# Kernel optimization log

Hardware: AMD Instinct MI355X
Metric: run time of the kernel (lower is better)

## Reference

```python
import jax, jax.numpy as jnp
import numpy as np

N_NODES = 50000
N_EDGES = 800000
IN_NF = 64
OUT_NF = 64
HID = 128
H = 4
D = 64
HD = H * D
EDGE_IN = 2 * IN_NF + 1 + 6   # 135
MSG_IN = HID + 1 + 3 + 6      # 138


def _p(key, i, shape, scale=0.02):
    return scale * jax.random.normal(jax.random.fold_in(key, i), shape, dtype=jnp.float32)


def setup_inputs() -> dict:
    key = jax.random.key(0)
    ks = jax.random.split(key, 4)
    inp = {
        "h": jax.random.normal(ks[0], (N_NODES, IN_NF), dtype=jnp.float32),
        "x": jax.random.normal(ks[1], (N_NODES, 3), dtype=jnp.float32),
        "edge_index": jax.random.randint(ks[2], (2, N_EDGES), 0, N_NODES, dtype=jnp.int32),
        "mask": jnp.ones((N_EDGES,), dtype=bool),
    }
    pk = jax.random.fold_in(key, 7)
    i = iter(range(100))
    inp.update({
        "Wq": _p(pk, next(i), (IN_NF, HD)), "bq": jnp.zeros((HD,)),
        "Wk": _p(pk, next(i), (IN_NF, HD)), "bk": jnp.zeros((HD,)),
        "Wv": _p(pk, next(i), (IN_NF, HD)), "bv": jnp.zeros((HD,)),
        "Wo": _p(pk, next(i), (HD, OUT_NF)), "bo": jnp.zeros((OUT_NF,)),
        "pw1": _p(pk, next(i), (1, HID // 2)), "pb1": jnp.zeros((HID // 2,)),
        "pw2": _p(pk, next(i), (HID // 2, H)), "pb2": jnp.zeros((H,)),
        "ew1": _p(pk, next(i), (EDGE_IN, HID)), "eb1": jnp.zeros((HID,)),
        "ew2": _p(pk, next(i), (HID, HID)), "eb2": jnp.zeros((HID,)),
        "eww": _p(pk, next(i), (HID, H)), "ewb": jnp.zeros((H,)),
        "mw1": _p(pk, next(i), (MSG_IN, HID)), "mb1": jnp.zeros((HID,)),
        "mw2": _p(pk, next(i), (HID, HID)), "mb2": jnp.zeros((HID,)),
        "gw": _p(pk, next(i), (HID, H)), "gb": jnp.zeros((H,)),
        "cw1": _p(pk, next(i), (HID, HID)), "cb1": jnp.zeros((HID,)),
        "cw2": _p(pk, next(i), (HID, H)), "cb2": jnp.zeros((H,)),
        "coord_weights": jnp.ones((H,)),
        "xw1": _p(pk, next(i), (HID, HID)), "xb1": jnp.zeros((HID,)),
        "xw2": _p(pk, next(i), (HID, H)), "xb2": jnp.zeros((H,)),
    })
    return inp


def reference(h, x, edge_index, mask,
              Wq, bq, Wk, bk, Wv, bv, Wo, bo,
              pw1, pb1, pw2, pb2,
              ew1, eb1, ew2, eb2, eww, ewb,
              mw1, mb1, mw2, mb2,
              gw, gb, cw1, cb1, cw2, cb2,
              coord_weights, xw1, xb1, xw2, xb2):
    silu = jax.nn.silu
    row, col = edge_index[0], edge_index[1]
    n = h.shape[0]

    q = (h @ Wq + bq).reshape(n, H, D)
    k = (h @ Wk + bk).reshape(n, H, D)
    v = (h @ Wv + bv).reshape(n, H, D)

    rel_pos = x[row] - x[col]                         # [E,3]
    rel_dist = jnp.sum(rel_pos ** 2, -1, keepdims=True)  # [E,1]
    pos_enc = silu(rel_dist @ pw1 + pb1) @ pw2 + pb2     # [E,H]

    # torch .std() is unbiased (ddof=1)
    xn = (x - x.mean(0, keepdims=True)) / (jnp.std(x, 0, keepdims=True, ddof=1) + 1e-8)

    edge_attr = jnp.concatenate([h[row], h[col], rel_dist, xn[row], xn[col]], -1)
    ef = silu(edge_attr @ ew1 + eb1) @ ew2 + eb2      # [E,HID]
    ewt = ef @ eww + ewb                              # [E,H]

    attn = jnp.einsum('ehd,ehd->eh', q[row], k[col]) / jnp.sqrt(jnp.float32(D))
    attn = attn + pos_enc + ewt
    attn = jnp.where(mask[:, None], attn, jnp.float32(-1e9))

    amax = jax.ops.segment_max(attn, row, num_segments=n)   # [N,H]
    attn = jnp.exp(attn - amax[row])
    asum = jax.ops.segment_sum(attn, row, num_segments=n)
    attn = attn / (asum[row] + 1e-8)                         # [E,H]

    msg_in = jnp.concatenate([ef, attn.mean(1, keepdims=True), rel_pos, xn[row], xn[col]], -1)
    msgs = silu(msg_in @ mw1 + mb1) @ mw2 + mb2              # [E,HID]

    gates = jax.nn.sigmoid(msgs @ gw + gb)                   # [E,H]
    cwts = silu(msgs @ cw1 + cb1) @ cw2 + cb2                # [E,H]

    # per-head index_add into the same buffer == sum over heads of the scalar weight
    s = jnp.sum(gates * cwts * coord_weights, -1, keepdims=True)  # [E,1]
    base = 0.9 * rel_pos + 0.1 * x[col]
    coord_update = jax.ops.segment_sum(s * base / (n - 1), row, num_segments=n)

    cross_v = jnp.cross(rel_pos, jnp.roll(rel_pos, 1, axis=0))
    cg = silu(msgs @ xw1 + xb1) @ xw2 + xb2                  # [E,H]
    cross_s = jnp.sum(cg, -1, keepdims=True)
    coord_update = coord_update + jax.ops.segment_sum(cross_s * cross_v / (n - 1), row, num_segments=n)

    wv = jax.ops.segment_sum(attn[..., None] * v[col], row, num_segments=n)  # [N,H,D]
    out = wv.reshape(n, HD) @ Wo + bo
    return out, coord_update
```

## Files before the change

### kernel.cpp

```cpp
#include <hip/hip_runtime.h>
#include <hip/hip_bf16.h>

#define NN 50000
#define NE 800000

typedef __bf16 bf16x8 __attribute__((ext_vector_type(8)));
typedef float f4v __attribute__((ext_vector_type(4)));

__device__ __forceinline__ float silu_f(float v){
  return v*__builtin_amdgcn_rcpf(1.0f+__expf(-v));
}
__device__ __forceinline__ float bf2f(unsigned int u){ return __uint_as_float(u<<16); }
__device__ __forceinline__ unsigned bfr(float f){
  unsigned b = __float_as_uint(f);
  return b + 0x7fffu + ((b>>16)&1u);
}
__device__ __forceinline__ unsigned short f2bf(float f){ return (unsigned short)(bfr(f)>>16); }
__device__ __forceinline__ unsigned pk2(float a, float b){
  unsigned r;
  asm("v_cvt_pk_bf16_f32 %0, %1, %2" : "=v"(r) : "v"(a), "v"(b));
  return r;
}

union U8 { unsigned short us[8]; uint4 u4; };

__device__ __forceinline__ void pack8(unsigned short* dst, float4 a, float4 b){
  uint4 u;
  u.x = pk2(a.x,a.y); u.y = pk2(a.z,a.w);
  u.z = pk2(b.x,b.y); u.w = pk2(b.z,b.w);
  *(uint4*)dst = u;
}

__device__ __forceinline__ int lidx(int e, int c, int CH){
  return (e*CH + ((c & ~7) | ((c ^ e) & 7))) << 3;
}

template<int KC, int CH>
__device__ __forceinline__ void gemm_rm(const unsigned short* act, const unsigned short* wf,
                                        int wu, int lane, f4v (&acc)[4][2]){
  int le = lane & 15, quad = lane >> 4;
  #pragma unroll
  for (int kc=0;kc<KC;kc++){
    bf16x8 a0 = *(const bf16x8*)(wf + (((wu*2  )*KC + kc)<<9) + lane*8);
    bf16x8 a1 = *(const bf16x8*)(wf + (((wu*2+1)*KC + kc)<<9) + lane*8);
    int chunk = kc*4 + quad;
    #pragma unroll
    for (int et=0;et<4;et++){
      bf16x8 b = *(const bf16x8*)(act + lidx(et*16+le, chunk, CH));
      acc[et][0] = __builtin_amdgcn_mfma_f32_16x16x32_bf16(a0, b, acc[et][0], 0,0,0);
      acc[et][1] = __builtin_amdgcn_mfma_f32_16x16x32_bf16(a1, b, acc[et][1], 0,0,0);
    }
  }
}

template<int CH, bool SILU, bool BIAS>
__device__ __forceinline__ void epi_rm(unsigned short* dst, const f4v (&acc)[4][2],
                                       const float* bias, int wu, int lane){
  int le = lane & 15, quad = lane >> 4;
  #pragma unroll
  for (int ot=0; ot<2; ot++){
    float4 bv = make_float4(0,0,0,0);
    if (BIAS) bv = *(const float4*)(bias + wu*32 + ot*16 + quad*4);
    int chunk = wu*4 + ot*2 + (quad>>1);
    int soff = (quad&1)*4;
    #pragma unroll
    for (int et=0; et<4; et++){
      float v0=acc[et][ot][0], v1=acc[et][ot][1], v2=acc[et][ot][2], v3=acc[et][ot][3];
      if (BIAS){ v0+=bv.x; v1+=bv.y; v2+=bv.z; v3+=bv.w; }
      if (SILU){ v0=silu_f(v0); v1=silu_f(v1); v2=silu_f(v2); v3=silu_f(v3); }
      uint2 u; u.x = pk2(v0,v1); u.y = pk2(v2,v3);
      *(uint2*)(dst + lidx(et*16+le, chunk, CH) + soff) = u;
    }
  }
}

template<int CH>
__device__ __forceinline__ void mfma_head(const unsigned short* buf, const unsigned short* whf,
                                          int wu, int lane, float* dst ){
  int le = lane & 15, quad = lane >> 4;
  f4v hacc = {0.f,0.f,0.f,0.f};
  #pragma unroll
  for (int kc=0;kc<4;kc++){
    bf16x8 a = *(const bf16x8*)(whf + (kc<<9) + lane*8);
    bf16x8 b = *(const bf16x8*)(buf + lidx(wu*16+le, kc*4+quad, CH));
    hacc = __builtin_amdgcn_mfma_f32_16x16x32_bf16(a, b, hacc, 0,0,0);
  }
  if (quad==0){
    #pragma unroll
    for (int r=0;r<4;r++) dst[r*65 + wu*16 + le] = hacc[r];
  }
}

__global__ __launch_bounds__(256) void k_zero(float* __restrict__ p, int n){
  int i = blockIdx.x*256 + threadIdx.x;
  if (i < n) p[i] = 0.f;
}

__global__ __launch_bounds__(256) void k_wcomb(const float* __restrict__ ew2, const float* __restrict__ eww,
                                               const float* __restrict__ eb2, const float* __restrict__ ewb,
                                               const float* __restrict__ pb2,
                                               float* __restrict__ wcomb, float* __restrict__ stats){
  int t = threadIdx.x;
  #pragma unroll
  for (int o=t;o<512;o+=256){
    int i=o>>2, hh=o&3;
    float s=0.f;
    for (int j=0;j<128;j++) s += ew2[i*128+j]*eww[j*4+hh];
    wcomb[o]=s;
  }
  if (t<4){
    float s=0.f;
    for (int j=0;j<128;j++) s += eb2[j]*eww[j*4+t];
    stats[12+t] = s + ewb[t] + pb2[t];
  }
}

__global__ __launch_bounds__(256) void k_wprep(const float* __restrict__ src, unsigned short* __restrict__ dst,
                                               int Kreal, int KC){
  int idx = blockIdx.x*256 + threadIdx.x;
  int tot = 8*KC*512;
  if (idx >= tot) return;
  int nt  = idx/(KC*512); int rem = idx%(KC*512);
  int kc  = rem>>9;       int r2  = rem&511;
  int lq  = r2>>3;        int j   = r2&7;
  int k   = kc*32 + (lq>>4)*8 + j;
  int n   = nt*16 + (lq&15);
  float v = (k < Kreal) ? src[k*128 + n] : 0.f;
  dst[idx] = f2bf(v);
}

__global__ __launch_bounds__(256) void k_wprepq(const float* __restrict__ src, unsigned short* __restrict__ dst){
  int idx = blockIdx.x*256 + threadIdx.x;
  if (idx >= 16384) return;
  int nt  = idx>>10;  int rem = idx&1023;
  int kc  = rem>>9;   int r2  = rem&511;
  int lq  = r2>>3;    int j   = r2&7;
  int k   = kc*32 + (lq>>4)*8 + j;
  int n   = nt*16 + (lq&15);
  dst[idx] = f2bf(src[k*256 + n]);
}

__global__ __launch_bounds__(256) void k_wprep4(const float* __restrict__ src, unsigned short* __restrict__ dst){
  int idx = blockIdx.x*256 + threadIdx.x;
  if (idx >= 2048) return;
  int kc = idx>>9; int r2 = idx&511; int lq = r2>>3; int j = r2&7;
  int k = kc*32 + (lq>>4)*8 + j;
  int n = lq&15;
  dst[idx] = f2bf((n<4) ? src[k*4+n] : 0.f);
}

__global__ __launch_bounds__(256) void k_stats(const float* __restrict__ x, float* __restrict__ stats){
  int i = blockIdx.x*256 + threadIdx.x;
  float v0=0.f,v1=0.f,v2=0.f;
  if (i < NN){ v0=x[i*3+0]; v1=x[i*3+1]; v2=x[i*3+2]; }
  float vals[6] = {v0,v1,v2,v0*v0,v1*v1,v2*v2};
  __shared__ float red[256];
  for (int c=0;c<6;c++){
    red[threadIdx.x]=vals[c];
    __syncthreads();
    for (int off=128; off>0; off>>=1){
      if (threadIdx.x < off) red[threadIdx.x] += red[threadIdx.x+off];
      __syncthreads();
    }
    if (threadIdx.x==0) atomicAdd(&stats[c], red[0]);
    __syncthreads();
  }
}

__global__ __launch_bounds__(64) void k_statsfin(float* __restrict__ stats){
  int t = threadIdx.x;
  if (t < 3){
    float s = stats[t], sq = stats[3+t];
    float mean = s/(float)NN;
    float var = (sq - s*s/(float)NN)/(float)(NN-1);
    float sd = sqrtf(var);
    stats[6+t] = mean;
    stats[9+t] = 1.0f/(sd + 1e-8f);
  }
}

__global__ __launch_bounds__(256) void k_qkv2(const float* __restrict__ h,
    const unsigned short* __restrict__ wqf,
    const float* __restrict__ bq, const float* __restrict__ bk, const float* __restrict__ bv,
    unsigned short* __restrict__ q, unsigned short* __restrict__ kk, unsigned short* __restrict__ v){
  __shared__ __align__(16) unsigned short hstage[64*8*8];
  int t = threadIdx.x; int lane = t & 63; int w = t >> 6;
  int wu = __builtin_amdgcn_readfirstlane(w);
  int r0 = blockIdx.x*64;
  {
    int row = r0 + lane;
    float4 a = make_float4(0,0,0,0), b2 = make_float4(0,0,0,0),
           c = make_float4(0,0,0,0), d2 = make_float4(0,0,0,0);
    if (row < NN){
      const float* hr = h + (size_t)row*64 + wu*16;
      a  = *(const float4*)(hr);    b2 = *(const float4*)(hr+4);
      c  = *(const float4*)(hr+8);  d2 = *(const float4*)(hr+12);
    }
    pack8(&hstage[lidx(lane, 2*wu,   8)], a, b2);
    pack8(&hstage[lidx(lane, 2*wu+1, 8)], c, d2);
  }
  __syncthreads();
  int le = lane & 15, quad = lane >> 4;
  #pragma unroll
  for (int ti=0; ti<12; ti++){
    int tt = ti*4 + wu;
    f4v acc[4];
    f4v z = {0.f,0.f,0.f,0.f};
    acc[0]=z; acc[1]=z; acc[2]=z; acc[3]=z;
    #pragma unroll
    for (int kc=0;kc<2;kc++){
      bf16x8 a = *(const bf16x8*)(wqf + ((tt*2 + kc)<<9) + lane*8);
      int chunk = kc*4 + quad;
      #pragma unroll
      for (int et=0;et<4;et++){
        bf16x8 b = *(const bf16x8*)(hstage + lidx(et*16+le, chunk, 8));
        acc[et] = __builtin_amdgcn_mfma_f32_16x16x32_bf16(a, b, acc[et], 0,0,0);
      }
    }
    int mat = tt>>4; int ct = tt&15;
    const float* bias = (mat==0)? bq : (mat==1)? bk : bv;
    unsigned short* outp = (mat==0)? q : (mat==1)? kk : v;
    float4 bv4 = *(const float4*)(bias + ct*16 + quad*4);
    int col = ct*16 + quad*4;
    #pragma unroll
    for (int et=0;et<4;et++){
      int row2 = r0 + et*16 + le;
      if (row2 < NN){
        float v0=acc[et][0]+bv4.x, v1=acc[et][1]+bv4.y, v2=acc[et][2]+bv4.z, v3=acc[et][3]+bv4.w;
        if (mat<2){
          uint2 u; u.x = pk2(v0,v1); u.y = pk2(v2,v3);
          *(uint2*)(outp + (size_t)row2*256 + col) = u;
        } else {
          int head = col>>6, dd = col&63;
          unsigned short* vp = outp + (size_t)row2*256 + (size_t)dd*4 + head;
          vp[0]  = f2bf(v0);
          vp[4]  = f2bf(v1);
          vp[8]  = f2bf(v2);
          vp[12] = f2bf(v3);
        }
      }
    }
  }
}

__global__ __launch_bounds__(256) void k_count(const int* __restrict__ ei, int* __restrict__ counts){
  int e = blockIdx.x*256 + threadIdx.x;
  if (e < NE) atomicAdd(&counts[ei[e]], 1);
}

__global__ __launch_bounds__(256) void k_scan(int* __restrict__ counts, int* __restrict__ offs){
  __shared__ int ps[256];
  int t = threadIdx.x;
  int base = t*196;
  int s = 0;
  for (int i=0;i<196;i++){ int idx = base+i; if (idx < NN) s += counts[idx]; }
  ps[t]=s; __syncthreads();
  for (int off=1; off<256; off<<=1){
    int vv = (t>=off)? ps[t-off] : 0;
    __syncthreads();
    ps[t]+=vv;
    __syncthreads();
  }
  int run = ps[t]-s;
  for (int i=0;i<196;i++){
    int idx = base+i;
    if (idx < NN){ int c = counts[idx]; offs[idx]=run; counts[idx]=run; run+=c; }
  }
  if (t==255) offs[NN]=run;
}

__global__ __launch_bounds__(256) void k_fill(const int* __restrict__ ei, int* __restrict__ cursor, int* __restrict__ elist){
  int e = blockIdx.x*256 + threadIdx.x;
  if (e < NE){
    int r = ei[e];
    int p = atomicAdd(&cursor[r],1);
    elist[p] = e;
  }
}

__global__ __launch_bounds__(256) void k_e1(
    const float* __restrict__ h, const float* __restrict__ x, const int* __restrict__ ei,
    const float* __restrict__ stats,
    const unsigned short* __restrict__ qb, const unsigned short* __restrict__ kb,
    const unsigned short* __restrict__ wfrag, const unsigned short* __restrict__ whfrag,
    const float* __restrict__ eb1,
    const float* __restrict__ pw1, const float* __restrict__ pb1,
    const float* __restrict__ pw2,
    float* __restrict__ asum, float* __restrict__ eattn){
  __shared__ __align__(16) unsigned short bufIn[64*24*8];
  __shared__ float logit_s[256];
  __shared__ float ewt2_s[4*65];
  __shared__ float pos_s[4*65];
  __shared__ float rd_s[64], xnr_s[192], xnc_s[192];
  __shared__ int row_s[64], col_s[64];
  int t = threadIdx.x; int lane = t & 63; int w = t >> 6;
  int wu = __builtin_amdgcn_readfirstlane(w);
  int ebase = blockIdx.x * 64;

  for (int i=t;i<260;i+=256) pos_s[i]=0.f;
  if (t < 64){
    int ge = ebase + t;
    int r = ei[ge], c = ei[NE+ge];
    row_s[t]=r; col_s[t]=c;
    float xr0=x[r*3],xr1=x[r*3+1],xr2=x[r*3+2];
    float xc0=x[c*3],xc1=x[c*3+1],xc2=x[c*3+2];
    float rp0=xr0-xc0, rp1=xr1-xc1, rp2=xr2-xc2;
    rd_s[t]=rp0*rp0+rp1*rp1+rp2*rp2;
    float m0=stats[6],m1=stats[7],m2=stats[8],s0=stats[9],s1=stats[10],s2=stats[11];
    xnr_s[t*3+0]=(xr0-m0)*s0; xnr_s[t*3+1]=(xr1-m1)*s1; xnr_s[t*3+2]=(xr2-m2)*s2;
    xnc_s[t*3+0]=(xc0-m0)*s0; xnc_s[t*3+1]=(xc1-m1)*s1; xnc_s[t*3+2]=(xc2-m2)*s2;
  }
  __syncthreads();

  for (int ii=0; ii<16; ii++){
    int e = wu*16+ii;
    int r = row_s[e], c = col_s[e];
    uint2 qu = *(const uint2*)(qb + (size_t)r*256 + lane*4);
    uint2 ku = *(const uint2*)(kb + (size_t)c*256 + lane*4);
    float d = bf2f(qu.x&0xffffu)*bf2f(ku.x&0xffffu)
            + bf2f(qu.x>>16)   *bf2f(ku.x>>16)
            + bf2f(qu.y&0xffffu)*bf2f(ku.y&0xffffu)
            + bf2f(qu.y>>16)   *bf2f(ku.y>>16);
    d += __shfl_xor(d,1,16); d += __shfl_xor(d,2,16);
    d += __shfl_xor(d,4,16); d += __shfl_xor(d,8,16);
    if ((lane&15)==0) logit_s[e*4 + (lane>>4)] = d*0.125f;
  }
  {
    int jb = wu*16;
    float rd = rd_s[lane];
    float p0=0,p1=0,p2=0,p3=0;
    for (int j=jb; j<jb+16; j++){
      float hp = rd*pw1[j] + pb1[j];
      float hs = silu_f(hp);
      const float4 w4 = *(const float4*)(pw2 + j*4);
      p0+=hs*w4.x; p1+=hs*w4.y; p2+=hs*w4.z; p3+=hs*w4.w;
    }
    atomicAdd(&pos_s[0*65+lane],p0);
    atomicAdd(&pos_s[1*65+lane],p1);
    atomicAdd(&pos_s[2*65+lane],p2);
    atomicAdd(&pos_s[3*65+lane],p3);
  }
  {
    const float* hr = h + (size_t)row_s[lane]*64 + wu*16;
    pack8(&bufIn[lidx(lane, 2*wu,   24)], *(const float4*)(hr),   *(const float4*)(hr+4));
    pack8(&bufIn[lidx(lane, 2*wu+1, 24)], *(const float4*)(hr+8), *(const float4*)(hr+12));
    const float* hc = h + (size_t)col_s[lane]*64 + wu*16;
    pack8(&bufIn[lidx(lane, 8+2*wu, 24)], *(const float4*)(hc),   *(const float4*)(hc+4));
    pack8(&bufIn[lidx(lane, 9+2*wu, 24)], *(const float4*)(hc+8), *(const float4*)(hc+12));
  }
  if (t < 64){
    pack8(&bufIn[lidx(t,16,24)],
          make_float4(rd_s[t], xnr_s[t*3+0], xnr_s[t*3+1], xnr_s[t*3+2]),
          make_float4(xnc_s[t*3+0], xnc_s[t*3+1], xnc_s[t*3+2], 0.f));
  }
  {
    uint4 z4 = make_uint4(0,0,0,0);
    int e = t&63, j = t>>6;
    if (j < 3) *(uint4*)&bufIn[lidx(e, 17+j, 24)] = z4;
  }
  __syncthreads();
  f4v acc[4][2];
  f4v z = {0.f,0.f,0.f,0.f};
  #pragma unroll
  for (int et=0;et<4;et++){ acc[et][0]=z; acc[et][1]=z; }
  gemm_rm<5,24>(bufIn, wfrag + 0, wu, lane, acc);
  __syncthreads();
  epi_rm<24,true,true>(bufIn, acc, eb1, wu, lane);
  __syncthreads();
  mfma_head<24>(bufIn, whfrag + 0, wu, lane, ewt2_s);
  __syncthreads();
  {
    int e2 = t>>2, hh = t&3;
    float lg = logit_s[t] + stats[12+hh] + ewt2_s[hh*65+e2] + pos_s[hh*65+e2];
    float ex = __expf(lg);
    eattn[(size_t)ebase*4 + t] = ex;
    atomicAdd(&asum[row_s[e2]*4 + hh], ex);
  }
}

__global__ __launch_bounds__(256) void k_e2(
    const float* __restrict__ h, const float* __restrict__ x, const int* __restrict__ ei,
    const float* __restrict__ stats,
    const float* __restrict__ asum, const float* __restrict__ eattn,
    const unsigned short* __restrict__ wfrag, const unsigned short* __restrict__ whfrag,
    const float* __restrict__ eb1, const float* __restrict__ eb2,
    const float* __restrict__ mb1, const float* __restrict__ mb2,
    const float* __restrict__ gb,
    const float* __restrict__ cb1, const float* __restrict__ cb2,
    const float* __restrict__ coordw,
    const float* __restrict__ xb1, const float* __restrict__ xb2,
    float* __restrict__ cvec){
  __shared__ __align__(16) unsigned short bufIn[64*24*8];
  __shared__ __align__(16) unsigned short bufA [64*16*8];
  __shared__ float attn_s[256];
  __shared__ float g_s[4*65], c_s[4*65], xx_s[4*65];
  __shared__ float s_s[64], cs_s[64];
  __shared__ float rp_s[192], rd_s[64], xnr_s[192], xnc_s[192], xc_s[192];
  __shared__ int row_s[64], col_s[64];
  int t = threadIdx.x; int lane = t & 63; int w = t >> 6;
  int wu = __builtin_amdgcn_readfirstlane(w);
  int ebase = blockIdx.x * 64;

  if (t < 64){
    int ge = ebase + t;
    int r = ei[ge], c = ei[NE+ge];
    row_s[t]=r; col_s[t]=c;
    float xr0=x[r*3],xr1=x[r*3+1],xr2=x[r*3+2];
    float xc0=x[c*3],xc1=x[c*3+1],xc2=x[c*3+2];
    float rp0=xr0-xc0, rp1=xr1-xc1, rp2=xr2-xc2;
    rp_s[t*3+0]=rp0; rp_s[t*3+1]=rp1; rp_s[t*3+2]=rp2;
    rd_s[t]=rp0*rp0+rp1*rp1+rp2*rp2;
    xc_s[t*3+0]=xc0; xc_s[t*3+1]=xc1; xc_s[t*3+2]=xc2;
    float m0=stats[6],m1=stats[7],m2=stats[8],s0=stats[9],s1=stats[10],s2=stats[11];
    xnr_s[t*3+0]=(xr0-m0)*s0; xnr_s[t*3+1]=(xr1-m1)*s1; xnr_s[t*3+2]=(xr2-m2)*s2;
    xnc_s[t*3+0]=(xc0-m0)*s0; xnc_s[t*3+1]=(xc1-m1)*s1; xnc_s[t*3+2]=(xc2-m2)*s2;
  }
  __syncthreads();
  {
    int e2 = t>>2; int hh = t&3;
    float ex = eattn[(size_t)ebase*4 + t];
    float a = ex / (asum[row_s[e2]*4 + hh] + 1e-8f);
    attn_s[t]=a;
  }
  {
    const float* hr = h + (size_t)row_s[lane]*64 + wu*16;
    pack8(&bufIn[lidx(lane, 2*wu,   24)], *(const float4*)(hr),   *(const float4*)(hr+4));
    pack8(&bufIn[lidx(lane, 2*wu+1, 24)], *(const float4*)(hr+8), *(const float4*)(hr+12));
    const float* hc = h + (size_t)col_s[lane]*64 + wu*16;
    pack8(&bufIn[lidx(lane, 8+2*wu, 24)], *(const float4*)(hc),   *(const float4*)(hc+4));
    pack8(&bufIn[lidx(lane, 9+2*wu, 24)], *(const float4*)(hc+8), *(const float4*)(hc+12));
  }
  if (t < 64){
    pack8(&bufIn[lidx(t,16,24)],
          make_float4(rd_s[t], xnr_s[t*3+0], xnr_s[t*3+1], xnr_s[t*3+2]),
          make_float4(xnc_s[t*3+0], xnc_s[t*3+1], xnc_s[t*3+2], 0.f));
  }
  {
    uint4 z4 = make_uint4(0,0,0,0);
    int e = t&63, j = t>>6;
    *(uint4*)&bufIn[lidx(e, 17+j, 24)] = z4;
    if (j < 3) *(uint4*)&bufIn[lidx(e, 21+j, 24)] = z4;
  }
  __syncthreads();
  f4v acc[4][2];
  f4v z = {0.f,0.f,0.f,0.f};
  #pragma unroll
  for (int et=0;et<4;et++){ acc[et][0]=z; acc[et][1]=z; }
  gemm_rm<5,24>(bufIn, wfrag + 0, wu, lane, acc);
  epi_rm<16,true,true>(bufA, acc, eb1, wu, lane);
  __syncthreads();
  #pragma unroll
  for (int et=0;et<4;et++){ acc[et][0]=z; acc[et][1]=z; }
  gemm_rm<4,16>(bufA, wfrag + 20480, wu, lane, acc);
  epi_rm<24,false,true>(bufIn, acc, eb2, wu, lane);
  if (t < 64){
    float am = 0.25f*(attn_s[t*4]+attn_s[t*4+1]+attn_s[t*4+2]+attn_s[t*4+3]);
    pack8(&bufIn[lidx(t,16,24)],
          make_float4(am, rp_s[t*3+0], rp_s[t*3+1], rp_s[t*3+2]),
          make_float4(xnr_s[t*3+0], xnr_s[t*3+1], xnr_s[t*3+2], xnc_s[t*3+0]));
    pack8(&bufIn[lidx(t,17,24)],
          make_float4(xnc_s[t*3+1], xnc_s[t*3+2], 0.f, 0.f),
          make_float4(0.f,0.f,0.f,0.f));
  }
  __syncthreads();
  #pragma unroll
  for (int et=0;et<4;et++){ acc[et][0]=z; acc[et][1]=z; }
  gemm_rm<5,24>(bufIn, wfrag + 36864, wu, lane, acc);
  epi_rm<16,true,true>(bufA, acc, mb1, wu, lane);
  __syncthreads();
  #pragma unroll
  for (int et=0;et<4;et++){ acc[et][0]=z; acc[et][1]=z; }
  gemm_rm<4,16>(bufA, wfrag + 57344, wu, lane, acc);
  epi_rm<24,false,true>(bufIn, acc, mb2, wu, lane);
  __syncthreads();
  mfma_head<24>(bufIn, whfrag + 2048, wu, lane, g_s);
  f4v ax[4][2];
  #pragma unroll
  for (int et=0;et<4;et++){ acc[et][0]=z; acc[et][1]=z; ax[et][0]=z; ax[et][1]=z; }
  {
    const unsigned short* wfc = wfrag + 73728;
    const unsigned short* wfx = wfrag + 90112;
    int le = lane&15, quad = lane>>4;
    #pragma unroll
    for (int kc=0;kc<4;kc++){
      bf16x8 ac0 = *(const bf16x8*)(wfc + (((wu*2  )*4 + kc)<<9) + lane*8);
      bf16x8 ac1 = *(const bf16x8*)(wfc + (((wu*2+1)*4 + kc)<<9) + lane*8);
      bf16x8 ax0 = *(const bf16x8*)(wfx + (((wu*2  )*4 + kc)<<9) + lane*8);
      bf16x8 ax1 = *(const bf16x8*)(wfx + (((wu*2+1)*4 + kc)<<9) + lane*8);
      int chunk = kc*4 + quad;
      #pragma unroll
      for (int et=0;et<4;et++){
        bf16x8 b = *(const bf16x8*)(bufIn + lidx(et*16+le, chunk, 24));
        acc[et][0] = __builtin_amdgcn_mfma_f32_16x16x32_bf16(ac0, b, acc[et][0], 0,0,0);
        acc[et][1] = __builtin_amdgcn_mfma_f32_16x16x32_bf16(ac1, b, acc[et][1], 0,0,0);
        ax[et][0]  = __builtin_amdgcn_mfma_f32_16x16x32_bf16(ax0, b, ax[et][0], 0,0,0);
        ax[et][1]  = __builtin_amdgcn_mfma_f32_16x16x32_bf16(ax1, b, ax[et][1], 0,0,0);
      }
    }
  }
  __syncthreads();
  epi_rm<16,true,true>(bufA, acc, cb1, wu, lane);
  epi_rm<24,true,true>(bufIn, ax, xb1, wu, lane);
  __syncthreads();
  mfma_head<16>(bufA, whfrag + 4096, wu, lane, c_s);
  mfma_head<24>(bufIn, whfrag + 6144, wu, lane, xx_s);
  __syncthreads();
  {
    int e2 = t>>2; int hh = t&3;
    float g = __builtin_amdgcn_rcpf(1.0f+__expf(-(g_s[hh*65+e2]+gb[hh])));
    float cwv = c_s[hh*65+e2]+cb2[hh];
    float sv = g*cwv*coordw[hh];
    float csv = xx_s[hh*65+e2]+xb2[hh];
    sv += __shfl_xor(sv,1);  sv += __shfl_xor(sv,2);
    csv += __shfl_xor(csv,1); csv += __shfl_xor(csv,2);
    if (hh==0){ s_s[e2]=sv; cs_s[e2]=csv; }
  }
  __syncthreads();
  if (t < 64){
    int ge = ebase + t;
    float rp0=rp_s[t*3],rp1=rp_s[t*3+1],rp2=rp_s[t*3+2];
    float pp0,pp1,pp2;
    if (t > 0){ pp0=rp_s[(t-1)*3]; pp1=rp_s[(t-1)*3+1]; pp2=rp_s[(t-1)*3+2]; }
    else {
      int gp = (ebase==0)? (NE-1) : (ebase-1);
      int rr=ei[gp], cc2=ei[NE+gp];
      pp0=x[rr*3]-x[cc2*3]; pp1=x[rr*3+1]-x[cc2*3+1]; pp2=x[rr*3+2]-x[cc2*3+2];
    }
    float cv0 = rp1*pp2 - rp2*pp1;
    float cv1 = rp2*pp0 - rp0*pp2;
    float cv2 = rp0*pp1 - rp1*pp0;
    float sv = s_s[t], csv = cs_s[t];
    const float inv = 1.0f/49999.0f;
    cvec[(size_t)ge*3+0] = (sv*(0.9f*rp0+0.1f*xc_s[t*3+0]) + csv*cv0)*inv;
    cvec[(size_t)ge*3+1] = (sv*(0.9f*rp1+0.1f*xc_s[t*3+1]) + csv*cv1)*inv;
    cvec[(size_t)ge*3+2] = (sv*(0.9f*rp2+0.1f*xc_s[t*3+2]) + csv*cv2)*inv;
  }
}

__global__ __launch_bounds__(256) void k_aggout(
    const int* __restrict__ ei, const int* __restrict__ offs, const int* __restrict__ elist,
    const float* __restrict__ eattn, const unsigned short* __restrict__ vb,
    const float* __restrict__ cvec, const float* __restrict__ Wo, const float* __restrict__ bo,
    const float* __restrict__ asum,
    float* __restrict__ outp){
  __shared__ float wvs[4*256];
  int t = threadIdx.x; int lane = t & 63; int w = t >> 6;
  int node = blockIdx.x*4 + w;
  const int* colp = ei + NE;
  int s0 = offs[node], s1 = offs[node+1];
  float a0=0,a1=0,a2=0,a3=0,cc=0;
  int i = s0;
  for (; i+4<=s1; i+=4){
    int e0=elist[i], e1=elist[i+1], e2=elist[i+2], e3=elist[i+3];
    int c0=colp[e0], c1=colp[e1], c2=colp[e2], c3=colp[e3];
    uint2 v0 = *(const uint2*)(vb + (size_t)c0*256 + lane*4);
    uint2 v1 = *(const uint2*)(vb + (size_t)c1*256 + lane*4);
    uint2 v2 = *(const uint2*)(vb + (size_t)c2*256 + lane*4);
    uint2 v3 = *(const uint2*)(vb + (size_t)c3*256 + lane*4);
    float4 at0 = *(const float4*)(eattn + (size_t)e0*4);
    float4 at1 = *(const float4*)(eattn + (size_t)e1*4);
    float4 at2 = *(const float4*)(eattn + (size_t)e2*4);
    float4 at3 = *(const float4*)(eattn + (size_t)e3*4);
    if (lane < 3) cc += cvec[(size_t)e0*3+lane] + cvec[(size_t)e1*3+lane]
                      + cvec[(size_t)e2*3+lane] + cvec[(size_t)e3*3+lane];
    a0 += at0.x*bf2f(v0.x&0xffffu) + at1.x*bf2f(v1.x&0xffffu) + at2.x*bf2f(v2.x&0xffffu) + at3.x*bf2f(v3.x&0xffffu);
    a1 += at0.y*bf2f(v0.x>>16)     + at1.y*bf2f(v1.x>>16)     + at2.y*bf2f(v2.x>>16)     + at3.y*bf2f(v3.x>>16);
    a2 += at0.z*bf2f(v0.y&0xffffu) + at1.z*bf2f(v1.y&0xffffu) + at2.z*bf2f(v2.y&0xffffu) + at3.z*bf2f(v3.y&0xffffu);
    a3 += at0.w*bf2f(v0.y>>16)     + at1.w*bf2f(v1.y>>16)     + at2.w*bf2f(v2.y>>16)     + at3.w*bf2f(v3.y>>16);
  }
  for (; i<s1; i++){
    int e0 = elist[i];
    int c0 = colp[e0];
    uint2 v0 = *(const uint2*)(vb + (size_t)c0*256 + lane*4);
    float4 at0 = *(const float4*)(eattn + (size_t)e0*4);
    if (lane < 3) cc += cvec[(size_t)e0*3+lane];
    a0 += at0.x*bf2f(v0.x&0xffffu);
    a1 += at0.y*bf2f(v0.x>>16);
    a2 += at0.z*bf2f(v0.y&0xffffu);
    a3 += at0.w*bf2f(v0.y>>16);
  }
  {
    const float* as = asum + (size_t)node*4;
    a0 /= (as[0] + 1e-8f);
    a1 /= (as[1] + 1e-8f);
    a2 /= (as[2] + 1e-8f);
    a3 /= (as[3] + 1e-8f);
  }
  wvs[w*256 +       lane]=a0;
  wvs[w*256 +  64 + lane]=a1;
  wvs[w*256 + 128 + lane]=a2;
  wvs[w*256 + 192 + lane]=a3;
  if (lane < 3) outp[(size_t)NN*64 + (size_t)node*3 + lane] = cc;
  float o = bo[lane];
  #pragma unroll 4
  for (int k2=0;k2<256;k2++) o += wvs[w*256+k2] * Wo[k2*64+lane];
  outp[(size_t)node*64 + lane] = o;
}

extern "C" void kernel_launch(void* const* d_in, const int* in_sizes, int n_in,
                              void* d_out, int out_size, void* d_ws, size_t ws_size,
                              hipStream_t stream) {
  const float* h  = (const float*)d_in[0];
  const float* x  = (const float*)d_in[1];
  const int*   ei = (const int*)d_in[2];
  const float* Wq=(const float*)d_in[4];  const float* bq=(const float*)d_in[5];
  const float* Wk=(const float*)d_in[6];  const float* bk=(const float*)d_in[7];
  const float* Wv=(const float*)d_in[8];  const float* bv=(const float*)d_in[9];
  const float* Wo=(const float*)d_in[10]; const float* bo=(const float*)d_in[11];
  const float* pw1=(const float*)d_in[12]; const float* pb1=(const float*)d_in[13];
  const float* pw2=(const float*)d_in[14]; const float* pb2=(const float*)d_in[15];
  const float* ew1=(const float*)d_in[16]; const float* eb1=(const float*)d_in[17];
  const float* ew2=(const float*)d_in[18]; const float* eb2=(const float*)d_in[19];
  const float* eww=(const float*)d_in[20]; const float* ewb=(const float*)d_in[21];
  const float* mw1=(const float*)d_in[22]; const float* mb1=(const float*)d_in[23];
  const float* mw2=(const float*)d_in[24]; const float* mb2=(const float*)d_in[25];
  const float* gw=(const float*)d_in[26];  const float* gb=(const float*)d_in[27];
  const float* cw1=(const float*)d_in[28]; const float* cb1=(const float*)d_in[29];
  const float* cw2=(const float*)d_in[30]; const float* cb2=(const float*)d_in[31];
  const float* coordw=(const float*)d_in[32];
  const float* xw1=(const float*)d_in[33]; const float* xb1=(const float*)d_in[34];
  const float* xw2=(const float*)d_in[35]; const float* xb2=(const float*)d_in[36];

  char* B = (char*)d_ws;
  float* eattn = (float*)(B + 0);
  float* cvec  = (float*)(B + 12800000);
  float* stats = (float*)(B + 22400000);
  float* asum  = (float*)(B + 22400064);
  int* counts  = (int*)(B + 23200064);
  int* offs    = (int*)(B + 23400064);
  unsigned short* wfrag = (unsigned short*)(B + 23600080);
  int* elist   = (int*)(B + 23813088);
  unsigned short* qb = (unsigned short*)(B + 27013088);
  unsigned short* kb = (unsigned short*)(B + 52613088);
  unsigned short* vb = (unsigned short*)(B + 78213088);
  unsigned short* whfrag = (unsigned short*)(B + 103813088);
  float* wcomb = (float*)elist;
  unsigned short* qkvf = (unsigned short*)eattn;

  k_zero<<<977,256,0,stream>>>(stats, 250016);
  k_wcomb<<<1,256,0,stream>>>(ew2, eww, eb2, ewb, pb2, wcomb, stats);
  k_wprep<<<80,256,0,stream>>>(ew1, wfrag + 0,     135, 5);
  k_wprep<<<64,256,0,stream>>>(ew2, wfrag + 20480, 128, 4);
  k_wprep<<<80,256,0,stream>>>(mw1, wfrag + 36864, 138, 5);
  k_wprep<<<64,256,0,stream>>>(mw2, wfrag + 57344, 128, 4);
  k_wprep<<<64,256,0,stream>>>(cw1, wfrag + 73728, 128, 4);
  k_wprep<<<64,256,0,stream>>>(xw1, wfrag + 90112, 128, 4);
  k_wprepq<<<64,256,0,stream>>>(Wq, qkvf + 0);
  k_wprepq<<<64,256,0,stream>>>(Wk, qkvf + 16384);
  k_wprepq<<<64,256,0,stream>>>(Wv, qkvf + 32768);
  k_wprep4<<<8,256,0,stream>>>(wcomb, whfrag + 0);
  k_wprep4<<<8,256,0,stream>>>(gw,  whfrag + 2048);
  k_wprep4<<<8,256,0,stream>>>(cw2, whfrag + 4096);
  k_wprep4<<<8,256,0,stream>>>(xw2, whfrag + 6144);

  k_stats<<<196,256,0,stream>>>(x, stats);
  k_statsfin<<<1,64,0,stream>>>(stats);
  k_qkv2<<<782,256,0,stream>>>(h, qkvf, bq, bk, bv, qb, kb, vb);
  k_count<<<3125,256,0,stream>>>(ei,counts);
  k_scan<<<1,256,0,stream>>>(counts,offs);
  k_fill<<<3125,256,0,stream>>>(ei,counts,elist);
  k_e1<<<12500,256,0,stream>>>(h,x,ei,stats,qb,kb,wfrag,whfrag,eb1,pw1,pb1,pw2,asum,eattn);
  k_e2<<<12500,256,0,stream>>>(h,x,ei,stats,asum,eattn,wfrag,whfrag,eb1,eb2,mb1,mb2,gb,cb1,cb2,coordw,xb1,xb2,cvec);
  k_aggout<<<12500,256,0,stream>>>(ei,offs,elist,eattn,vb,cvec,Wo,bo,asum,(float*)d_out);
}
```

Baseline: 1.237 ms.

## Fold linear layer pairs in edge kernel into precomposed weights

The second edge kernel's projections have no nonlinearity between them, so several pairs are folded on the device ahead of time: ew2 with mw1, and mw2 with each of gw, cw1 and xw1. Their biases are folded the same way. This removes two 128x128 per-edge GEMM stages, the intermediate shared buffer and some barriers from k_e2. The cost is four small setup kernels, a few extra barriers from the sequential head evaluations, and bf16 rounding of the composed weights instead of the originals.

```diff
diff --git a/kernel.cpp b/kernel.cpp
--- a/kernel.cpp
+++ b/kernel.cpp
@@ -112,6 +112,59 @@
     float s=0.f;
     for (int j=0;j<128;j++) s += eb2[j]*eww[j*4+t];
     stats[12+t] = s + ewb[t] + pb2[t];
+  }
+}
+
+__global__ __launch_bounds__(256) void k_wfold(const float* __restrict__ A, const float* __restrict__ Bm,
+                                               const float* __restrict__ abias, const float* __restrict__ b2,
+                                               float* __restrict__ dstW, float* __restrict__ dstB){
+  int idx = blockIdx.x*256 + threadIdx.x;
+  if (idx >= 129*128) return;
+  int i = idx>>7, n = idx&127;
+  if (i<128){
+    float s=0.f;
+    for (int j=0;j<128;j++) s += A[i*128+j]*Bm[j*128+n];
+    dstW[i*128+n]=s;
+  } else {
+    float s=b2[n];
+    for (int j=0;j<128;j++) s += abias[j]*Bm[j*128+n];
+    dstB[n]=s;
+  }
+}
+
+__global__ __launch_bounds__(256) void k_wfoldm(const float* __restrict__ ew2, const float* __restrict__ mw1,
+                                                const float* __restrict__ eb2, const float* __restrict__ mb1,
+                                                float* __restrict__ dstW, float* __restrict__ dstB){
+  int idx = blockIdx.x*256 + threadIdx.x;
+  if (idx >= 139*128) return;
+  int i = idx>>7, n = idx&127;
+  if (i<128){
+    float s=0.f;
+    for (int j=0;j<128;j++) s += ew2[i*128+j]*mw1[j*128+n];
+    dstW[i*128+n]=s;
+  } else if (i<138){
+    dstW[i*128+n] = mw1[i*128+n];
+  } else {
+    float s=mb1[n];
+    for (int j=0;j<128;j++) s += eb2[j]*mw1[j*128+n];
+    dstB[n]=s;
+  }
+}
+
+__global__ __launch_bounds__(256) void k_wfoldg(const float* __restrict__ mw2, const float* __restrict__ gw,
+                                                const float* __restrict__ mb2, const float* __restrict__ gb,
+                                                float* __restrict__ dstW, float* __restrict__ dstB){
+  int idx = blockIdx.x*256 + threadIdx.x;
+  if (idx >= 129*4) return;
+  int i = idx>>2, hh = idx&3;
+  if (i<128){
+    float s=0.f;
+    for (int j=0;j<128;j++) s += mw2[i*128+j]*gw[j*4+hh];
+    dstW[i*4+hh]=s;
+  } else {
+    float s=gb[hh];
+    for (int j=0;j<128;j++) s += mb2[j]*gw[j*4+hh];
+    dstB[hh]=s;
   }
 }
 
@@ -383,16 +436,12 @@
     const float* __restrict__ stats,
     const float* __restrict__ asum, const float* __restrict__ eattn,
     const unsigned short* __restrict__ wfrag, const unsigned short* __restrict__ whfrag,
-    const float* __restrict__ eb1, const float* __restrict__ eb2,
-    const float* __restrict__ mb1, const float* __restrict__ mb2,
-    const float* __restrict__ gb,
-    const float* __restrict__ cb1, const float* __restrict__ cb2,
-    const float* __restrict__ coordw,
-    const float* __restrict__ xb1, const float* __restrict__ xb2,
+    const float* __restrict__ eb1, const float* __restrict__ fbias,
+    const float* __restrict__ cb2, const float* __restrict__ coordw,
+    const float* __restrict__ xb2,
     float* __restrict__ cvec){
   __shared__ __align__(16) unsigned short bufIn[64*24*8];
-  __shared__ __align__(16) unsigned short bufA [64*16*8];
-  __shared__ float attn_s[256];
+  __shared__ float am_s[64];
   __shared__ float g_s[4*65], c_s[4*65], xx_s[4*65];
   __shared__ float s_s[64], cs_s[64];
   __shared__ float rp_s[192], rd_s[64], xnr_s[192], xnc_s[192], xc_s[192];
@@ -420,7 +469,8 @@
     int e2 = t>>2; int hh = t&3;
     float ex = eattn[(size_t)ebase*4 + t];
     float a = ex / (asum[row_s[e2]*4 + hh] + 1e-8f);
-    attn_s[t]=a;
+    a += __shfl_xor(a,1); a += __shfl_xor(a,2);
+    if (hh==0) am_s[e2] = 0.25f*a;
   }
   {
     const float* hr = h + (size_t)row_s[lane]*64 + wu*16;
@@ -438,8 +488,7 @@
   {
     uint4 z4 = make_uint4(0,0,0,0);
     int e = t&63, j = t>>6;
-    *(uint4*)&bufIn[lidx(e, 17+j, 24)] = z4;
-    if (j < 3) *(uint4*)&bufIn[lidx(e, 21+j, 24)] = z4;
+    if (j < 3) *(uint4*)&bufIn[lidx(e, 17+j, 24)] = z4;
   }
   __syncthreads();
   f4v acc[4][2];
@@ -447,16 +496,11 @@
   #pragma unroll
   for (int et=0;et<4;et++){ acc[et][0]=z; acc[et][1]=z; }
   gemm_rm<5,24>(bufIn, wfrag + 0, wu, lane, acc);
-  epi_rm<16,true,true>(bufA, acc, eb1, wu, lane);
-  __syncthreads();
-  #pragma unroll
-  for (int et=0;et<4;et++){ acc[et][0]=z; acc[et][1]=z; }
-  gemm_rm<4,16>(bufA, wfrag + 20480, wu, lane, acc);
-  epi_rm<24,false,true>(bufIn, acc, eb2, wu, lane);
+  __syncthreads();
+  epi_rm<24,true,true>(bufIn, acc, eb1, wu, lane);
   if (t < 64){
-    float am = 0.25f*(attn_s[t*4]+attn_s[t*4+1]+attn_s[t*4+2]+attn_s[t*4+3]);
     pack8(&bufIn[lidx(t,16,24)],
-          make_float4(am, rp_s[t*3+0], rp_s[t*3+1], rp_s[t*3+2]),
+          make_float4(am_s[t], rp_s[t*3+0], rp_s[t*3+1], rp_s[t*3+2]),
           make_float4(xnr_s[t*3+0], xnr_s[t*3+1], xnr_s[t*3+2], xnc_s[t*3+0]));
     pack8(&bufIn[lidx(t,17,24)],
           make_float4(xnc_s[t*3+1], xnc_s[t*3+2], 0.f, 0.f),
@@ -465,21 +509,17 @@
   __syncthreads();
   #pragma unroll
   for (int et=0;et<4;et++){ acc[et][0]=z; acc[et][1]=z; }
-  gemm_rm<5,24>(bufIn, wfrag + 36864, wu, lane, acc);
-  epi_rm<16,true,true>(bufA, acc, mb1, wu, lane);
-  __syncthreads();
-  #pragma unroll
-  for (int et=0;et<4;et++){ acc[et][0]=z; acc[et][1]=z; }
-  gemm_rm<4,16>(bufA, wfrag + 57344, wu, lane, acc);
-  epi_rm<24,false,true>(bufIn, acc, mb2, wu, lane);
+  gemm_rm<5,24>(bufIn, wfrag + 20480, wu, lane, acc);
+  __syncthreads();
+  epi_rm<24,true,true>(bufIn, acc, fbias + 0, wu, lane);
   __syncthreads();
   mfma_head<24>(bufIn, whfrag + 2048, wu, lane, g_s);
   f4v ax[4][2];
   #pragma unroll
   for (int et=0;et<4;et++){ acc[et][0]=z; acc[et][1]=z; ax[et][0]=z; ax[et][1]=z; }
   {
-    const unsigned short* wfc = wfrag + 73728;
-    const unsigned short* wfx = wfrag + 90112;
+    const unsigned short* wfc = wfrag + 40960;
+    const unsigned short* wfx = wfrag + 57344;
     int le = lane&15, quad = lane>>4;
     #pragma unroll
     for (int kc=0;kc<4;kc++){
@@ -499,15 +539,17 @@
     }
   }
   __syncthreads();
-  epi_rm<16,true,true>(bufA, acc, cb1, wu, lane);
-  epi_rm<24,true,true>(bufIn, ax, xb1, wu, lane);
-  __syncthreads();
-  mfma_head<16>(bufA, whfrag + 4096, wu, lane, c_s);
+  epi_rm<24,true,true>(bufIn, acc, fbias + 128, wu, lane);
+  __syncthreads();
+  mfma_head<24>(bufIn, whfrag + 4096, wu, lane, c_s);
+  __syncthreads();
+  epi_rm<24,true,true>(bufIn, ax, fbias + 256, wu, lane);
+  __syncthreads();
   mfma_head<24>(bufIn, whfrag + 6144, wu, lane, xx_s);
   __syncthreads();
   {
     int e2 = t>>2; int hh = t&3;
-    float g = __builtin_amdgcn_rcpf(1.0f+__expf(-(g_s[hh*65+e2]+gb[hh])));
+    float g = __builtin_amdgcn_rcpf(1.0f+__expf(-(g_s[hh*65+e2]+fbias[384+hh])));
     float cwv = c_s[hh*65+e2]+cb2[hh];
     float sv = g*cwv*coordw[hh];
     float csv = xx_s[hh*65+e2]+xb2[hh];
@@ -634,22 +676,29 @@
   unsigned short* kb = (unsigned short*)(B + 52613088);
   unsigned short* vb = (unsigned short*)(B + 78213088);
   unsigned short* whfrag = (unsigned short*)(B + 103813088);
+  float* fbias = (float*)(wfrag + 73728);
   float* wcomb = (float*)elist;
+  float* wgf   = wcomb + 512;
+  float* wmf   = wgf + 512;
+  float* wcf   = wmf + 17664;
+  float* wxf   = wcf + 16384;
   unsigned short* qkvf = (unsigned short*)eattn;
 
   k_zero<<<977,256,0,stream>>>(stats, 250016);
   k_wcomb<<<1,256,0,stream>>>(ew2, eww, eb2, ewb, pb2, wcomb, stats);
+  k_wfoldm<<<70,256,0,stream>>>(ew2, mw1, eb2, mb1, wmf, fbias + 0);
+  k_wfold<<<65,256,0,stream>>>(mw2, cw1, mb2, cb1, wcf, fbias + 128);
+  k_wfold<<<65,256,0,stream>>>(mw2, xw1, mb2, xb1, wxf, fbias + 256);
+  k_wfoldg<<<3,256,0,stream>>>(mw2, gw, mb2, gb, wgf, fbias + 384);
   k_wprep<<<80,256,0,stream>>>(ew1, wfrag + 0,     135, 5);
-  k_wprep<<<64,256,0,stream>>>(ew2, wfrag + 20480, 128, 4);
-  k_wprep<<<80,256,0,stream>>>(mw1, wfrag + 36864, 138, 5);
-  k_wprep<<<64,256,0,stream>>>(mw2, wfrag + 57344, 128, 4);
-  k_wprep<<<64,256,0,stream>>>(cw1, wfrag + 73728, 128, 4);
-  k_wprep<<<64,256,0,stream>>>(xw1, wfrag + 90112, 128, 4);
+  k_wprep<<<80,256,0,stream>>>(wmf, wfrag + 20480, 138, 5);
+  k_wprep<<<64,256,0,stream>>>(wcf, wfrag + 40960, 128, 4);
+  k_wprep<<<64,256,0,stream>>>(wxf, wfrag + 57344, 128, 4);
   k_wprepq<<<64,256,0,stream>>>(Wq, qkvf + 0);
   k_wprepq<<<64,256,0,stream>>>(Wk, qkvf + 16384);
   k_wprepq<<<64,256,0,stream>>>(Wv, qkvf + 32768);
   k_wprep4<<<8,256,0,stream>>>(wcomb, whfrag + 0);
-  k_wprep4<<<8,256,0,stream>>>(gw,  whfrag + 2048);
+  k_wprep4<<<8,256,0,stream>>>(wgf, whfrag + 2048);
   k_wprep4<<<8,256,0,stream>>>(cw2, whfrag + 4096);
   k_wprep4<<<8,256,0,stream>>>(xw2, whfrag + 6144);
 
@@ -660,6 +709,6 @@
   k_scan<<<1,256,0,stream>>>(counts,offs);
   k_fill<<<3125,256,0,stream>>>(ei,counts,elist);
   k_e1<<<12500,256,0,stream>>>(h,x,ei,stats,qb,kb,wfrag,whfrag,eb1,pw1,pb1,pw2,asum,eattn);
-  k_e2<<<12500,256,0,stream>>>(h,x,ei,stats,asum,eattn,wfrag,whfrag,eb1,eb2,mb1,mb2,gb,cb1,cb2,coordw,xb1,xb2,cvec);
+  k_e2<<<12500,256,0,stream>>>(h,x,ei,stats,asum,eattn,wfrag,whfrag,eb1,fbias,cb2,coordw,xb2,cvec);
   k_aggout<<<12500,256,0,stream>>>(ei,offs,elist,eattn,vb,cvec,Wo,bo,asum,(float*)d_out);
 }
```

New measurement: 1.313 ms. +6.1%, slower.
